# Kernel optimization log

Hardware: AMD Instinct MI355X
Metric: run time of the kernel (lower is better)

The kernel has to match this reference:

```python
import jax, jax.numpy as jnp
import numpy as np

EPS = 1e-8  # torch.nn.CosineSimilarity default eps


def _one_sided_chamfer(ex, ey):
    # ex: [N, D], ey: [M, D]
    # cosine(ex_i, ey_j) = <ex_i, ey_j> / (max(||ex_i||, eps) * max(||ey_j||, eps))
    nx = jnp.maximum(jnp.linalg.norm(ex, axis=-1, keepdims=True), EPS)  # [N,1]
    ny = jnp.maximum(jnp.linalg.norm(ey, axis=-1, keepdims=True), EPS)  # [M,1]
    exn = ex / nx
    eyn = ey / ny
    sims = jnp.einsum('nd,md->nm', exn, eyn)  # [N, M] cosine matrix
    return jnp.max(sims, axis=-1)  # row-wise max -> [N]


def setup_inputs() -> dict:
    key = jax.random.key(0)
    k1, k2 = jax.random.split(key)
    ex = jax.random.normal(k1, (8192, 768), dtype=jnp.float32)
    ey = jax.random.normal(k2, (8192, 768), dtype=jnp.float32)
    return {"ex": ex, "ey": ey}


def reference(ex, ey):
    return _one_sided_chamfer(ex, ey)
```

## Files before the change

kernel.cpp:

```cpp
#include <hip/hip_runtime.h>
#include <math.h>

#define NROWS 8192
#define KDIM  768
#define BM 128
#define BN 128
#define BKB 128
#define KTILES (KDIM / BKB)
#define NBC 2
#define NBCG (NROWS / BN / NBC)

typedef int i32x4 __attribute__((ext_vector_type(4)));

static __device__ __forceinline__ unsigned enc_f(float f) {
    unsigned x = __float_as_uint(f);
    return (x & 0x80000000u) ? ~x : (x | 0x80000000u);
}
static __device__ __forceinline__ float dec_f(unsigned u) {
    unsigned x = (u & 0x80000000u) ? (u ^ 0x80000000u) : ~u;
    return __uint_as_float(x);
}

__global__ __launch_bounds__(256) void normalize_quant_k(
        const float* __restrict__ ex, const float* __restrict__ ey,
        signed char* __restrict__ q, float* __restrict__ scales,
        unsigned* __restrict__ out) {
    if (blockIdx.x < NROWS / 256)
        out[blockIdx.x * 256 + threadIdx.x] = enc_f(-INFINITY);
    const int wave = threadIdx.x >> 6, lane = threadIdx.x & 63;
    const int grow = blockIdx.x * 4 + wave;
    const float* src = (grow < NROWS) ? ex : ey;
    const int row = grow & (NROWS - 1);
    const float4* xr = (const float4*)(src + (size_t)row * KDIM);
    float4 v[3];
    #pragma unroll
    for (int g = 0; g < 3; ++g) v[g] = xr[lane + g * 64];
    float ss = 0.f, am = 0.f;
    #pragma unroll
    for (int g = 0; g < 3; ++g) {
        ss += v[g].x * v[g].x + v[g].y * v[g].y + v[g].z * v[g].z + v[g].w * v[g].w;
        am = fmaxf(am, fmaxf(fmaxf(fabsf(v[g].x), fabsf(v[g].y)),
                             fmaxf(fabsf(v[g].z), fabsf(v[g].w))));
    }
    #pragma unroll
    for (int off = 32; off > 0; off >>= 1) {
        ss += __shfl_xor(ss, off);
        am = fmaxf(am, __shfl_xor(am, off));
    }
    const float scale = 1.0f / fmaxf(sqrtf(ss), 1e-8f);
    am = fmaxf(am * scale, 1e-12f);
    if (lane == 0) scales[grow] = am * (1.0f / 127.0f);
    const float si = scale * (127.0f / am);
    int* dr = (int*)(q + (size_t)grow * KDIM);
    #pragma unroll
    for (int g = 0; g < 3; ++g) {
        int qx = min(127, max(-127, __float2int_rn(v[g].x * si)));
        int qy = min(127, max(-127, __float2int_rn(v[g].y * si)));
        int qz = min(127, max(-127, __float2int_rn(v[g].z * si)));
        int qw = min(127, max(-127, __float2int_rn(v[g].w * si)));
        dr[lane + g * 64] = (qx & 0xff) | ((qy & 0xff) << 8) |
                            ((qz & 0xff) << 16) | ((qw & 0xff) << 24);
    }
}

__global__ __launch_bounds__(256, 5) void gemm_rowmax_i8_k(
        const signed char* __restrict__ A, const signed char* __restrict__ B,
        const float* __restrict__ sa, const float* __restrict__ sb,
        unsigned* __restrict__ out) {
    __shared__ signed char As[BM * BKB];
    __shared__ signed char Bs[BN * BKB];

    const int tid  = threadIdx.x;
    const int wave = tid >> 6, lane = tid & 63;
    const int xcd = blockIdx.x & 7;
    const int idx = blockIdx.x >> 3;
    const int br  = (xcd >> 1) * 16 + (idx & 15);
    const int bcg = (xcd & 1) * 16 + (idx >> 4);

    const int srow   = lane >> 3;
    const int gchunk = (lane & 7) ^ srow;
    const int scol   = gchunk * 16;
    const signed char* aStage = A + (size_t)(br * BM + wave * 8 + srow) * KDIM + scol;
    signed char* lA = As + wave * 1024;
    signed char* lB = Bs + wave * 1024;

    const int wm = (wave >> 1) * 64, wn = (wave & 1) * 64;
    const int quad = lane >> 4, mrow = lane & 15;
    const int c0 = quad ^ (mrow & 7);
    const signed char* aBase = As + (wm + mrow) * BKB;
    const signed char* bBase = Bs + (wn + mrow) * BKB;
    const int row0 = br * BM + wm + quad * 4;

    float rm[4][4];
    #pragma unroll
    for (int mi = 0; mi < 4; ++mi)
        #pragma unroll
        for (int r = 0; r < 4; ++r) rm[mi][r] = -INFINITY;

    #pragma unroll 1
    for (int bi = 0; bi < NBC; ++bi) {
        const int bc = bcg * NBC + bi;
        const signed char* bStage =
            B + (size_t)(bc * BN + wave * 8 + srow) * KDIM + scol;

        i32x4 acc[4][4] = {};

        #pragma unroll 1
        for (int kt = 0; kt < KTILES; ++kt) {
            __syncthreads();
            #pragma unroll
            for (int i = 0; i < 4; ++i) {
                __builtin_amdgcn_global_load_lds(
                    (const __attribute__((address_space(1))) void*)(aStage + kt * BKB + i * 24576),
                    (__attribute__((address_space(3))) void*)(lA + i * 4096), 16, 0, 0);
                __builtin_amdgcn_global_load_lds(
                    (const __attribute__((address_space(1))) void*)(bStage + kt * BKB + i * 24576),
                    (__attribute__((address_space(3))) void*)(lB + i * 4096), 16, 0, 0);
            }
            __syncthreads();

            #pragma unroll 1
            for (int ks = 0; ks < 2; ++ks) {
                const int ck = c0 ^ (ks << 2);
                i32x4 af[4], bfr[4];
                #pragma unroll
                for (int mi = 0; mi < 4; ++mi)
                    af[mi] = *(const i32x4*)(aBase + mi * 16 * BKB + ck * 16);
                #pragma unroll
                for (int ni = 0; ni < 4; ++ni)
                    bfr[ni] = *(const i32x4*)(bBase + ni * 16 * BKB + ck * 16);
                #pragma unroll
                for (int mi = 0; mi < 4; ++mi)
                    #pragma unroll
                    for (int ni = 0; ni < 4; ++ni)
                        acc[mi][ni] = __builtin_amdgcn_mfma_i32_16x16x64_i8(
                            af[mi], bfr[ni], acc[mi][ni], 0, 0, 0);
            }
        }

        float sbv[4];
        #pragma unroll
        for (int ni = 0; ni < 4; ++ni)
            sbv[ni] = sb[bc * BN + wn + ni * 16 + mrow];
        #pragma unroll
        for (int mi = 0; mi < 4; ++mi) {
            #pragma unroll
            for (int r = 0; r < 4; ++r) {
                float v = fmaxf(fmaxf((float)acc[mi][0][r] * sbv[0],
                                      (float)acc[mi][1][r] * sbv[1]),
                                fmaxf((float)acc[mi][2][r] * sbv[2],
                                      (float)acc[mi][3][r] * sbv[3]));
                rm[mi][r] = fmaxf(rm[mi][r], v);
            }
        }
    }

    #pragma unroll
    for (int mi = 0; mi < 4; ++mi) {
        #pragma unroll
        for (int r = 0; r < 4; ++r) {
            float v = rm[mi][r];
            v = fmaxf(v, __shfl_xor(v, 1));
            v = fmaxf(v, __shfl_xor(v, 2));
            v = fmaxf(v, __shfl_xor(v, 4));
            v = fmaxf(v, __shfl_xor(v, 8));
            if (mrow == 0) {
                const int row = row0 + mi * 16 + r;
                atomicMax(&out[row], enc_f(v * sa[row]));
            }
        }
    }
}

__global__ void decode_out_k(unsigned* __restrict__ u) {
    int i = blockIdx.x * 256 + threadIdx.x;
    ((float*)u)[i] = dec_f(u[i]);
}

extern "C" void kernel_launch(void* const* d_in, const int* in_sizes, int n_in,
                              void* d_out, int out_size, void* d_ws, size_t ws_size,
                              hipStream_t stream) {
    (void)in_sizes; (void)n_in; (void)out_size; (void)ws_size;
    const float* ex = (const float*)d_in[0];
    const float* ey = (const float*)d_in[1];
    signed char* q = (signed char*)d_ws;
    float* scales  = (float*)(q + 2 * (size_t)NROWS * KDIM);
    unsigned* outu = (unsigned*)d_out;

    normalize_quant_k<<<(2 * NROWS) / 4, 256, 0, stream>>>(ex, ey, q, scales, outu);
    gemm_rowmax_i8_k<<<(NROWS / BM) * NBCG, 256, 0, stream>>>(
        q, q + (size_t)NROWS * KDIM, scales, scales + NROWS, outu);
    decode_out_k<<<NROWS / 256, 256, 0, stream>>>(outu);
}
```

Baseline: 166.8 us.

## Fuse normalize, GEMM row-max and decode into one persistent kernel with grid barriers

Merges the three kernels into a single launch of 1024 blocks that normalize and quantize rows, meet at a software grid barrier, run the int8 GEMM with row-max, then meet again before decoding the output. NBC is raised from 2 to 4 so the block count drops and all blocks can be co-resident, which the spin barrier needs. This removes two kernel launches and their gaps. In exchange it adds a memset launch, atomic spin barriers, and fewer GEMM blocks, each doing more column tiles. It can deadlock if not all blocks fit on the device at once.

```diff
diff --git a/kernel.cpp b/kernel.cpp
--- a/kernel.cpp
+++ b/kernel.cpp
@@ -7,8 +7,9 @@
 #define BN 128
 #define BKB 128
 #define KTILES (KDIM / BKB)
-#define NBC 2
+#define NBC 4
 #define NBCG (NROWS / BN / NBC)
+#define NBLK ((NROWS / BM) * NBCG)
 
 typedef int i32x4 __attribute__((ext_vector_type(4)));
 
@@ -21,61 +22,87 @@
     return __uint_as_float(x);
 }
 
-__global__ __launch_bounds__(256) void normalize_quant_k(
+static __device__ __forceinline__ void grid_barrier(unsigned* cnt, unsigned* gen) {
+    __syncthreads();
+    if (threadIdx.x == 0) {
+        __threadfence();
+        const unsigned g = __hip_atomic_load(gen, __ATOMIC_ACQUIRE,
+                                             __HIP_MEMORY_SCOPE_AGENT);
+        const unsigned a = __hip_atomic_fetch_add(cnt, 1u, __ATOMIC_ACQ_REL,
+                                                  __HIP_MEMORY_SCOPE_AGENT);
+        if (a == NBLK - 1) {
+            __hip_atomic_store(cnt, 0u, __ATOMIC_RELAXED, __HIP_MEMORY_SCOPE_AGENT);
+            __hip_atomic_fetch_add(gen, 1u, __ATOMIC_RELEASE, __HIP_MEMORY_SCOPE_AGENT);
+        } else {
+            while (__hip_atomic_load(gen, __ATOMIC_ACQUIRE,
+                                     __HIP_MEMORY_SCOPE_AGENT) == g)
+                __builtin_amdgcn_s_sleep(2);
+        }
+        __threadfence();
+    }
+    __syncthreads();
+}
+
+__global__ __launch_bounds__(256, 4) void fused_cosine_k(
         const float* __restrict__ ex, const float* __restrict__ ey,
         signed char* __restrict__ q, float* __restrict__ scales,
-        unsigned* __restrict__ out) {
-    if (blockIdx.x < NROWS / 256)
-        out[blockIdx.x * 256 + threadIdx.x] = enc_f(-INFINITY);
-    const int wave = threadIdx.x >> 6, lane = threadIdx.x & 63;
-    const int grow = blockIdx.x * 4 + wave;
-    const float* src = (grow < NROWS) ? ex : ey;
-    const int row = grow & (NROWS - 1);
-    const float4* xr = (const float4*)(src + (size_t)row * KDIM);
-    float4 v[3];
-    #pragma unroll
-    for (int g = 0; g < 3; ++g) v[g] = xr[lane + g * 64];
-    float ss = 0.f, am = 0.f;
-    #pragma unroll
-    for (int g = 0; g < 3; ++g) {
-        ss += v[g].x * v[g].x + v[g].y * v[g].y + v[g].z * v[g].z + v[g].w * v[g].w;
-        am = fmaxf(am, fmaxf(fmaxf(fabsf(v[g].x), fabsf(v[g].y)),
-                             fmaxf(fabsf(v[g].z), fabsf(v[g].w))));
-    }
-    #pragma unroll
-    for (int off = 32; off > 0; off >>= 1) {
-        ss += __shfl_xor(ss, off);
-        am = fmaxf(am, __shfl_xor(am, off));
-    }
-    const float scale = 1.0f / fmaxf(sqrtf(ss), 1e-8f);
-    am = fmaxf(am * scale, 1e-12f);
-    if (lane == 0) scales[grow] = am * (1.0f / 127.0f);
-    const float si = scale * (127.0f / am);
-    int* dr = (int*)(q + (size_t)grow * KDIM);
-    #pragma unroll
-    for (int g = 0; g < 3; ++g) {
-        int qx = min(127, max(-127, __float2int_rn(v[g].x * si)));
-        int qy = min(127, max(-127, __float2int_rn(v[g].y * si)));
-        int qz = min(127, max(-127, __float2int_rn(v[g].z * si)));
-        int qw = min(127, max(-127, __float2int_rn(v[g].w * si)));
-        dr[lane + g * 64] = (qx & 0xff) | ((qy & 0xff) << 8) |
-                            ((qz & 0xff) << 16) | ((qw & 0xff) << 24);
-    }
-}
-
-__global__ __launch_bounds__(256, 5) void gemm_rowmax_i8_k(
-        const signed char* __restrict__ A, const signed char* __restrict__ B,
-        const float* __restrict__ sa, const float* __restrict__ sb,
-        unsigned* __restrict__ out) {
+        unsigned* __restrict__ out, unsigned* bar) {
     __shared__ signed char As[BM * BKB];
     __shared__ signed char Bs[BN * BKB];
 
     const int tid  = threadIdx.x;
     const int wave = tid >> 6, lane = tid & 63;
+
+    if (blockIdx.x < NROWS / 256)
+        out[blockIdx.x * 256 + tid] = enc_f(-INFINITY);
+    #pragma unroll 1
+    for (int g = 0; g < 4; ++g) {
+        const int grow = g * 4096 + blockIdx.x * 4 + wave;
+        const float* src = (grow < NROWS) ? ex : ey;
+        const int row = grow & (NROWS - 1);
+        const float4* xr = (const float4*)(src + (size_t)row * KDIM);
+        float4 v[3];
+        #pragma unroll
+        for (int c = 0; c < 3; ++c) v[c] = xr[lane + c * 64];
+        float ss = 0.f, am = 0.f;
+        #pragma unroll
+        for (int c = 0; c < 3; ++c) {
+            ss += v[c].x * v[c].x + v[c].y * v[c].y + v[c].z * v[c].z + v[c].w * v[c].w;
+            am = fmaxf(am, fmaxf(fmaxf(fabsf(v[c].x), fabsf(v[c].y)),
+                                 fmaxf(fabsf(v[c].z), fabsf(v[c].w))));
+        }
+        #pragma unroll
+        for (int off = 32; off > 0; off >>= 1) {
+            ss += __shfl_xor(ss, off);
+            am = fmaxf(am, __shfl_xor(am, off));
+        }
+        const float scale = 1.0f / fmaxf(sqrtf(ss), 1e-8f);
+        am = fmaxf(am * scale, 1e-12f);
+        if (lane == 0) scales[grow] = am * (1.0f / 127.0f);
+        const float si = scale * (127.0f / am);
+        int* dr = (int*)(q + (size_t)grow * KDIM);
+        #pragma unroll
+        for (int c = 0; c < 3; ++c) {
+            int qx = min(127, max(-127, __float2int_rn(v[c].x * si)));
+            int qy = min(127, max(-127, __float2int_rn(v[c].y * si)));
+            int qz = min(127, max(-127, __float2int_rn(v[c].z * si)));
+            int qw = min(127, max(-127, __float2int_rn(v[c].w * si)));
+            dr[lane + c * 64] = (qx & 0xff) | ((qy & 0xff) << 8) |
+                                ((qz & 0xff) << 16) | ((qw & 0xff) << 24);
+        }
+    }
+
+    grid_barrier(bar, bar + 1);
+
+    const signed char* A = q;
+    const signed char* B = q + (size_t)NROWS * KDIM;
+    const float* sa = scales;
+    const float* sb = scales + NROWS;
+
     const int xcd = blockIdx.x & 7;
     const int idx = blockIdx.x >> 3;
     const int br  = (xcd >> 1) * 16 + (idx & 15);
-    const int bcg = (xcd & 1) * 16 + (idx >> 4);
+    const int bcg = (xcd & 1) * 8 + (idx >> 4);
 
     const int srow   = lane >> 3;
     const int gchunk = (lane & 7) ^ srow;
@@ -170,11 +197,14 @@
             }
         }
     }
-}
-
-__global__ void decode_out_k(unsigned* __restrict__ u) {
-    int i = blockIdx.x * 256 + threadIdx.x;
-    ((float*)u)[i] = dec_f(u[i]);
+
+    grid_barrier(bar, bar + 1);
+
+    if (blockIdx.x < NROWS / 256) {
+        const int i = blockIdx.x * 256 + tid;
+        const unsigned u = out[i];
+        ((float*)out)[i] = dec_f(u);
+    }
 }
 
 extern "C" void kernel_launch(void* const* d_in, const int* in_sizes, int n_in,
@@ -185,10 +215,9 @@
     const float* ey = (const float*)d_in[1];
     signed char* q = (signed char*)d_ws;
     float* scales  = (float*)(q + 2 * (size_t)NROWS * KDIM);
+    unsigned* bar  = (unsigned*)(scales + 2 * NROWS);
     unsigned* outu = (unsigned*)d_out;
 
-    normalize_quant_k<<<(2 * NROWS) / 4, 256, 0, stream>>>(ex, ey, q, scales, outu);
-    gemm_rowmax_i8_k<<<(NROWS / BM) * NBCG, 256, 0, stream>>>(
-        q, q + (size_t)NROWS * KDIM, scales, scales + NROWS, outu);
-    decode_out_k<<<NROWS / 256, 256, 0, stream>>>(outu);
-}
+    hipMemsetAsync(bar, 0, 2 * sizeof(unsigned), stream);
+    fused_cosine_k<<<NBLK, 256, 0, stream>>>(ex, ey, q, scales, outu, bar);
+}
```

Result: slower. 565.8 us (+239.2%).

## Load MFMA fragments directly from global memory and fuse decode via last-block ticket

Applied to the files above, without the earlier changes.

The int8 GEMM drops LDS staging and its barriers, with each wave loading its MFMA operand fragments straight from global memory (relying on L2/cache reuse). Each block now covers 4 column tiles instead of 2, halving the grid, and launch bounds go from 5 to 4 blocks per SM. The separate decode kernel is replaced by a ticket counter, so the last finishing block decodes the output, and a memset resets the ticket each call. Skipping LDS removes sync overhead, but it gives up shared-memory reuse across waves and makes the global loads less coalesced.

```diff
diff --git a/kernel.cpp b/kernel.cpp
--- a/kernel.cpp
+++ b/kernel.cpp
@@ -5,10 +5,10 @@
 #define KDIM  768
 #define BM 128
 #define BN 128
-#define BKB 128
-#define KTILES (KDIM / BKB)
-#define NBC 2
+#define KT12 (KDIM / 64)
+#define NBC 4
 #define NBCG (NROWS / BN / NBC)
+#define NBLK ((NROWS / BM) * NBCG)
 
 typedef int i32x4 __attribute__((ext_vector_type(4)));
 
@@ -63,33 +63,23 @@
     }
 }
 
-__global__ __launch_bounds__(256, 5) void gemm_rowmax_i8_k(
+__global__ __launch_bounds__(256, 4) void gemm_rowmax_i8_k(
         const signed char* __restrict__ A, const signed char* __restrict__ B,
         const float* __restrict__ sa, const float* __restrict__ sb,
-        unsigned* __restrict__ out) {
-    __shared__ signed char As[BM * BKB];
-    __shared__ signed char Bs[BN * BKB];
-
+        unsigned* __restrict__ out, unsigned* __restrict__ ticket) {
     const int tid  = threadIdx.x;
     const int wave = tid >> 6, lane = tid & 63;
     const int xcd = blockIdx.x & 7;
     const int idx = blockIdx.x >> 3;
     const int br  = (xcd >> 1) * 16 + (idx & 15);
-    const int bcg = (xcd & 1) * 16 + (idx >> 4);
-
-    const int srow   = lane >> 3;
-    const int gchunk = (lane & 7) ^ srow;
-    const int scol   = gchunk * 16;
-    const signed char* aStage = A + (size_t)(br * BM + wave * 8 + srow) * KDIM + scol;
-    signed char* lA = As + wave * 1024;
-    signed char* lB = Bs + wave * 1024;
+    const int bcg = (xcd & 1) * 8 + (idx >> 4);
 
     const int wm = (wave >> 1) * 64, wn = (wave & 1) * 64;
     const int quad = lane >> 4, mrow = lane & 15;
-    const int c0 = quad ^ (mrow & 7);
-    const signed char* aBase = As + (wm + mrow) * BKB;
-    const signed char* bBase = Bs + (wn + mrow) * BKB;
     const int row0 = br * BM + wm + quad * 4;
+
+    const signed char* aP =
+        A + (size_t)(br * BM + wm + mrow) * KDIM + quad * 16;
 
     float rm[4][4];
     #pragma unroll
@@ -100,42 +90,26 @@
     #pragma unroll 1
     for (int bi = 0; bi < NBC; ++bi) {
         const int bc = bcg * NBC + bi;
-        const signed char* bStage =
-            B + (size_t)(bc * BN + wave * 8 + srow) * KDIM + scol;
+        const signed char* bP =
+            B + (size_t)(bc * BN + wn + mrow) * KDIM + quad * 16;
 
         i32x4 acc[4][4] = {};
 
-        #pragma unroll 1
-        for (int kt = 0; kt < KTILES; ++kt) {
-            __syncthreads();
+        #pragma unroll 2
+        for (int kt = 0; kt < KT12; ++kt) {
+            i32x4 af[4], bfr[4];
             #pragma unroll
-            for (int i = 0; i < 4; ++i) {
-                __builtin_amdgcn_global_load_lds(
-                    (const __attribute__((address_space(1))) void*)(aStage + kt * BKB + i * 24576),
-                    (__attribute__((address_space(3))) void*)(lA + i * 4096), 16, 0, 0);
-                __builtin_amdgcn_global_load_lds(
-                    (const __attribute__((address_space(1))) void*)(bStage + kt * BKB + i * 24576),
-                    (__attribute__((address_space(3))) void*)(lB + i * 4096), 16, 0, 0);
-            }
-            __syncthreads();
-
-            #pragma unroll 1
-            for (int ks = 0; ks < 2; ++ks) {
-                const int ck = c0 ^ (ks << 2);
-                i32x4 af[4], bfr[4];
-                #pragma unroll
-                for (int mi = 0; mi < 4; ++mi)
-                    af[mi] = *(const i32x4*)(aBase + mi * 16 * BKB + ck * 16);
+            for (int mi = 0; mi < 4; ++mi)
+                af[mi] = *(const i32x4*)(aP + (size_t)mi * 16 * KDIM + kt * 64);
+            #pragma unroll
+            for (int ni = 0; ni < 4; ++ni)
+                bfr[ni] = *(const i32x4*)(bP + (size_t)ni * 16 * KDIM + kt * 64);
+            #pragma unroll
+            for (int mi = 0; mi < 4; ++mi)
                 #pragma unroll
                 for (int ni = 0; ni < 4; ++ni)
-                    bfr[ni] = *(const i32x4*)(bBase + ni * 16 * BKB + ck * 16);
-                #pragma unroll
-                for (int mi = 0; mi < 4; ++mi)
-                    #pragma unroll
-                    for (int ni = 0; ni < 4; ++ni)
-                        acc[mi][ni] = __builtin_amdgcn_mfma_i32_16x16x64_i8(
-                            af[mi], bfr[ni], acc[mi][ni], 0, 0, 0);
-            }
+                    acc[mi][ni] = __builtin_amdgcn_mfma_i32_16x16x64_i8(
+                        af[mi], bfr[ni], acc[mi][ni], 0, 0, 0);
         }
 
         float sbv[4];
@@ -170,11 +144,23 @@
             }
         }
     }
-}
 
-__global__ void decode_out_k(unsigned* __restrict__ u) {
-    int i = blockIdx.x * 256 + threadIdx.x;
-    ((float*)u)[i] = dec_f(u[i]);
+    __shared__ unsigned lastFlag;
+    __threadfence();
+    __syncthreads();
+    if (tid == 0)
+        lastFlag = (__hip_atomic_fetch_add(ticket, 1u, __ATOMIC_ACQ_REL,
+                                           __HIP_MEMORY_SCOPE_AGENT)
+                    == (unsigned)(NBLK - 1));
+    __syncthreads();
+    if (lastFlag) {
+        __threadfence();
+        for (int i = tid; i < NROWS; i += 256) {
+            const unsigned u = __hip_atomic_load(&out[i], __ATOMIC_RELAXED,
+                                                 __HIP_MEMORY_SCOPE_AGENT);
+            ((float*)out)[i] = dec_f(u);
+        }
+    }
 }
 
 extern "C" void kernel_launch(void* const* d_in, const int* in_sizes, int n_in,
@@ -185,10 +171,11 @@
     const float* ey = (const float*)d_in[1];
     signed char* q = (signed char*)d_ws;
     float* scales  = (float*)(q + 2 * (size_t)NROWS * KDIM);
+    unsigned* ticket = (unsigned*)(scales + 2 * NROWS);
     unsigned* outu = (unsigned*)d_out;
 
+    hipMemsetAsync(ticket, 0, sizeof(unsigned), stream);
     normalize_quant_k<<<(2 * NROWS) / 4, 256, 0, stream>>>(ex, ey, q, scales, outu);
-    gemm_rowmax_i8_k<<<(NROWS / BM) * NBCG, 256, 0, stream>>>(
-        q, q + (size_t)NROWS * KDIM, scales, scales + NROWS, outu);
-    decode_out_k<<<NROWS / 256, 256, 0, stream>>>(outu);
+    gemm_rowmax_i8_k<<<NBLK, 256, 0, stream>>>(
+        q, q + (size_t)NROWS * KDIM, scales, scales + NROWS, outu, ticket);
 }
```

After: 341.4 us. +104.6%, slower.
